# Performance work log

Measured on AMD Instinct MI355X. Metric: run time of the kernel, lower is better.

Reference implementation:

```python
import jax, jax.numpy as jnp
import numpy as np

HEADS = 16
HEAD_DIM = 64
EMBED = HEADS * HEAD_DIM  # 1024
B, S = 2, 2048


def setup_inputs() -> dict:
    key = jax.random.key(0)
    ks = jax.random.split(key, 9)
    return {
        "value": jax.random.normal(ks[0], (B, S, EMBED), dtype=jnp.float32),
        "key": jax.random.normal(ks[1], (B, S, EMBED), dtype=jnp.float32),
        "query": jax.random.normal(ks[2], (B, S, EMBED), dtype=jnp.float32),
        "mask": jax.random.randint(ks[3], (B, 1, S, S), 0, 2, dtype=jnp.int32),
        "Wq": jax.random.normal(ks[4], (HEAD_DIM, HEAD_DIM), dtype=jnp.float32) * 0.02,
        "Wk": jax.random.normal(ks[5], (HEAD_DIM, HEAD_DIM), dtype=jnp.float32) * 0.02,
        "Wv": jax.random.normal(ks[6], (HEAD_DIM, HEAD_DIM), dtype=jnp.float32) * 0.02,
        "Wo": jax.random.normal(ks[7], (EMBED, EMBED), dtype=jnp.float32) * 0.02,
        "bo": jnp.zeros((EMBED,), dtype=jnp.float32),
    }


def reference(value, key, query, mask, Wq, Wk, Wv, Wo, bo):
    N, Lv = value.shape[0], value.shape[1]
    Lk, Lq = key.shape[1], query.shape[1]
    # Faithful to original: plain reshape (N, heads, len, head_dim), NOT transpose.
    v = value.reshape(N, HEADS, Lv, HEAD_DIM)
    k = key.reshape(N, HEADS, Lk, HEAD_DIM)
    q = query.reshape(N, HEADS, Lq, HEAD_DIM)
    # Per-head Linear (no bias): x @ W.T
    V = jnp.einsum('bhld,ed->bhle', v, Wv)
    K = jnp.einsum('bhld,ed->bhle', k, Wk)
    Q = jnp.einsum('bhld,ed->bhle', q, Wq)
    score = jnp.einsum('bhqd,bhkd->bhqk', Q, K)  # [B,H,Sq,Sk]
    score = jnp.where(mask == 0, jnp.float32(-1e20), score)
    # Faithful quirk: scale by sqrt(embed_size), not sqrt(head_dim)
    scale = jnp.float32(EMBED ** 0.5)
    attn = jax.nn.softmax(score / scale, axis=3)
    out = jnp.einsum('bhqk,bhkd->bhqd', attn, V).reshape(N, Lq, HEADS * HEAD_DIM)
    return out @ Wo.T + bo
```

## Files before the change

### kernel.cpp

```cpp
#include <hip/hip_runtime.h>
#include <hip/hip_bf16.h>
#include <cstdint>
#include <cstddef>

#define S_LEN 2048
#define N_HEADS 16
#define HD 64
#define EMB 1024
#define N_BATCH 2
#define N_BH (N_BATCH * N_HEADS)

typedef __attribute__((ext_vector_type(4))) float f32x4;
typedef __attribute__((ext_vector_type(8))) short short8;
typedef __attribute__((ext_vector_type(8))) _Float16 half8;
typedef __attribute__((ext_vector_type(2))) _Float16 half2v;

__device__ __forceinline__ f32x4 mfma16h(half8 a, half8 b, f32x4 c) {
    return __builtin_amdgcn_mfma_f32_16x16x32_f16(a, b, c, 0, 0, 0);
}

__device__ __forceinline__ unsigned pkh(float a, float b) {
    return __builtin_bit_cast(unsigned, __builtin_amdgcn_cvt_pkrtz(a, b));
}

#if __has_builtin(__builtin_amdgcn_exp2f)
__device__ __forceinline__ float fast_exp2(float x) { return __builtin_amdgcn_exp2f(x); }
#else
__device__ __forceinline__ float fast_exp2(float x) { return exp2f(x); }
#endif

__global__ __launch_bounds__(256) void prep_kernel(
    const float* __restrict__ q_in, const float* __restrict__ k_in,
    const float* __restrict__ v_in,
    const float* __restrict__ Wq, const float* __restrict__ Wk,
    const float* __restrict__ Wv, const float* __restrict__ Wo,
    const int* __restrict__ mask,
    short* __restrict__ Qb, short* __restrict__ Kb, short* __restrict__ Vt,
    short* __restrict__ Woh, unsigned long long* __restrict__ bits) {
    __shared__ short Al[64 * 72];
    __shared__ short Wl[64 * 72];
    __shared__ short Ol[64 * 72];
    int bx = blockIdx.x;
    int t = threadIdx.x;

    if (bx >= 3072) {
        if (bx < 11264) {
            int wid = ((bx - 3072) * 256 + t) >> 6;
            int lane = t & 63;
            const int* src = mask + (size_t)wid * 256 + lane;
            unsigned long long w0 = __ballot(src[0] != 0);
            unsigned long long w1 = __ballot(src[64] != 0);
            unsigned long long w2 = __ballot(src[128] != 0);
            unsigned long long w3 = __ballot(src[192] != 0);
            if (lane == 0) {
                unsigned long long* dst = bits + (size_t)wid * 4;
                dst[0] = w0; dst[1] = w1; dst[2] = w2; dst[3] = w3;
            }
        } else {
            int i = (bx - 11264) * 256 + t;
            f32x4 a = reinterpret_cast<const f32x4*>(Wo)[i * 2];
            f32x4 b = reinterpret_cast<const f32x4*>(Wo)[i * 2 + 1];
            uint4 u = { pkh(a.x, a.y), pkh(a.z, a.w), pkh(b.x, b.y), pkh(b.z, b.w) };
            reinterpret_cast<uint4*>(Woh)[i] = u;
        }
        return;
    }

    int rt = bx & 31;
    int bh = (bx >> 5) & 31;
    int tz = bx >> 10;
    const float* src = (tz == 0 ? q_in : tz == 1 ? k_in : v_in)
                       + (size_t)bh * S_LEN * HD + (size_t)rt * 64 * HD;
    const float* W = (tz == 0 ? Wq : tz == 1 ? Wk : Wv);

#pragma unroll
    for (int r = 0; r < 4; r++) {
        int f4 = t + 256 * r;
        int row = f4 >> 4;
        int c4 = (f4 & 15) * 4;
        f32x4 a = reinterpret_cast<const f32x4*>(src)[f4];
        uint2 ua = { pkh(a.x, a.y), pkh(a.z, a.w) };
        *reinterpret_cast<uint2*>(&Al[row * 72 + c4]) = ua;
        f32x4 w = reinterpret_cast<const f32x4*>(W)[f4];
        uint2 uw = { pkh(w.x, w.y), pkh(w.z, w.w) };
        *reinterpret_cast<uint2*>(&Wl[row * 72 + c4]) = uw;
    }
    __syncthreads();

    int wave = t >> 6, lane = t & 63, quad = lane >> 4, col = lane & 15;
    half8 a0 = *reinterpret_cast<const half8*>(&Al[(wave * 16 + col) * 72 + quad * 8]);
    half8 a1 = *reinterpret_cast<const half8*>(&Al[(wave * 16 + col) * 72 + 32 + quad * 8]);

    const float C1 = 0.04508422002777448f;
    float scl = (tz == 0) ? C1 : 1.0f;

    f32x4 acc[4];
#pragma unroll
    for (int jt = 0; jt < 4; jt++) {
        half8 b0 = *reinterpret_cast<const half8*>(&Wl[(jt * 16 + col) * 72 + quad * 8]);
        half8 b1 = *reinterpret_cast<const half8*>(&Wl[(jt * 16 + col) * 72 + 32 + quad * 8]);
        f32x4 c = {0.f, 0.f, 0.f, 0.f};
        c = mfma16h(a0, b0, c);
        c = mfma16h(a1, b1, c);
        acc[jt] = c;
    }
    __syncthreads();

    if (tz < 2) {
#pragma unroll
        for (int jt = 0; jt < 4; jt++)
#pragma unroll
            for (int i = 0; i < 4; i++)
                Ol[(wave * 16 + quad * 4 + i) * 72 + jt * 16 + col] =
                    __builtin_bit_cast(short, (_Float16)(acc[jt][i] * scl));
        __syncthreads();
        short* dst = (tz == 0 ? Qb : Kb) + (size_t)bh * S_LEN * HD + (size_t)rt * 64 * HD;
        int row = t >> 2, ck = (t & 3) * 16;
        short8 o0 = *reinterpret_cast<const short8*>(&Ol[row * 72 + ck]);
        short8 o1 = *reinterpret_cast<const short8*>(&Ol[row * 72 + ck + 8]);
        *reinterpret_cast<short8*>(&dst[row * 64 + ck]) = o0;
        *reinterpret_cast<short8*>(&dst[row * 64 + ck + 8]) = o1;
    } else {
#pragma unroll
        for (int jt = 0; jt < 4; jt++)
#pragma unroll
            for (int i = 0; i < 4; i++)
                Ol[(jt * 16 + col) * 72 + wave * 16 + quad * 4 + i] =
                    __builtin_bit_cast(short, (_Float16)acc[jt][i]);
        __syncthreads();
        short* dst = Vt + (size_t)bh * HD * S_LEN + rt * 64;
        int d = t >> 2, ck = (t & 3) * 16;
        short8 o0 = *reinterpret_cast<const short8*>(&Ol[d * 72 + ck]);
        short8 o1 = *reinterpret_cast<const short8*>(&Ol[d * 72 + ck + 8]);
        *reinterpret_cast<short8*>(&dst[(size_t)d * S_LEN + ck]) = o0;
        *reinterpret_cast<short8*>(&dst[(size_t)d * S_LEN + ck + 8]) = o1;
    }
}

__global__ __launch_bounds__(512, 4) void attn_kernel(
    const short* __restrict__ Qb, const short* __restrict__ Kb,
    const short* __restrict__ Vt, const unsigned long long* __restrict__ mbits,
    short* __restrict__ Xb) {
    int qt = blockIdx.x;
    int bh = blockIdx.y;
    int b = bh >> 4;
    int t = threadIdx.x, wave = t >> 6, lane = t & 63, quad = lane >> 4, col = lane & 15;
    int qg = wave & 3;
    int par = wave >> 2;

    __shared__ short smem[16384 + 8 * 32 * 72];
    short* Pl = smem + 16384;
    short* Pw = Pl + wave * (32 * 72);
    const short* Kp = smem + par * 4096;
    const short* Vp = smem + 8192 + par * 4096;

    const short* Qh = Qb + (size_t)bh * S_LEN * HD;
    const short* Kh = Kb + (size_t)bh * S_LEN * HD;
    const short* Vh = Vt + (size_t)bh * HD * S_LEN;
    int q0 = qt * 128 + qg * 32;

    half8 qf00 = *reinterpret_cast<const half8*>(&Qh[(size_t)(q0 + col) * HD + quad * 8]);
    half8 qf01 = *reinterpret_cast<const half8*>(&Qh[(size_t)(q0 + col) * HD + 32 + quad * 8]);
    half8 qf10 = *reinterpret_cast<const half8*>(&Qh[(size_t)(q0 + 16 + col) * HD + quad * 8]);
    half8 qf11 = *reinterpret_cast<const half8*>(&Qh[(size_t)(q0 + 16 + col) * HD + 32 + quad * 8]);

    const unsigned long long* mrow0 = mbits + (size_t)(b * S_LEN + q0 + col) * 32;
    const unsigned long long* mrow1 = mbits + (size_t)(b * S_LEN + q0 + 16 + col) * 32;

    int r0 = t >> 3, cc = t & 7;
    int dst0 = r0 * 64 + ((cc ^ (r0 & 7)) * 8);
    const short* kg0 = Kh + r0 * HD + cc * 8;
    const short* vg0 = Vh + (size_t)r0 * S_LEN + cc * 8;

    {
        short8 a = *reinterpret_cast<const short8*>(kg0);
        short8 b2 = *reinterpret_cast<const short8*>(kg0 + 4096);
        short8 c = *reinterpret_cast<const short8*>(vg0);
        short8 d = *reinterpret_cast<const short8*>(vg0 + 64);
        *reinterpret_cast<short8*>(&smem[dst0]) = a;
        *reinterpret_cast<short8*>(&smem[4096 + dst0]) = b2;
        *reinterpret_cast<short8*>(&smem[8192 + dst0]) = c;
        *reinterpret_cast<short8*>(&smem[12288 + dst0]) = d;
    }
    __syncthreads();

    unsigned bs[4];
#pragma unroll
    for (int i = 0; i < 4; i++) bs[i] = 1u << (quad * 4 + i);
    half8 ones = { (_Float16)1.f, (_Float16)1.f, (_Float16)1.f, (_Float16)1.f,
                   (_Float16)1.f, (_Float16)1.f, (_Float16)1.f, (_Float16)1.f };

    int sw = quad ^ (col & 7);
    unsigned long long mw0 = mrow0[par];
    unsigned long long mw1 = mrow1[par];

    f32x4 o[4][2];
    f32x4 l0 = {0.f, 0.f, 0.f, 0.f}, l1 = {0.f, 0.f, 0.f, 0.f};
#pragma unroll
    for (int dt = 0; dt < 4; dt++) {
        o[dt][0] = (f32x4){0.f, 0.f, 0.f, 0.f};
        o[dt][1] = (f32x4){0.f, 0.f, 0.f, 0.f};
    }

    for (int s = 0; s < 16; s++) {
        short8 pk0, pk1, pv0, pv1;
        unsigned long long mn0, mn1;
        if (s < 15) {
            pk0 = *reinterpret_cast<const short8*>(kg0 + (2 * s + 2) * 4096);
            pk1 = *reinterpret_cast<const short8*>(kg0 + (2 * s + 3) * 4096);
            pv0 = *reinterpret_cast<const short8*>(vg0 + (2 * s + 2) * 64);
            pv1 = *reinterpret_cast<const short8*>(vg0 + (2 * s + 3) * 64);
            mn0 = mrow0[2 * s + 2 + par];
            mn1 = mrow1[2 * s + 2 + par];
        }
#pragma unroll
        for (int mt = 0; mt < 4; mt++) {
            const short* kbase = &Kp[(mt * 16 + col) * 64];
            half8 ka0 = *reinterpret_cast<const half8*>(&kbase[sw * 8]);
            half8 ka1 = *reinterpret_cast<const half8*>(&kbase[(sw ^ 4) * 8]);
            f32x4 c0 = {0.f, 0.f, 0.f, 0.f};
            f32x4 c1 = {0.f, 0.f, 0.f, 0.f};
            c0 = mfma16h(ka0, qf00, c0);
            c0 = mfma16h(ka1, qf01, c0);
            c1 = mfma16h(ka0, qf10, c1);
            c1 = mfma16h(ka1, qf11, c1);
            unsigned g0 = (unsigned)(mw0 >> (mt * 16));
            unsigned g1 = (unsigned)(mw1 >> (mt * 16));
            float p00 = fast_exp2((g0 & bs[0]) ? c0[0] : -200.0f);
            float p01 = fast_exp2((g0 & bs[1]) ? c0[1] : -200.0f);
            float p02 = fast_exp2((g0 & bs[2]) ? c0[2] : -200.0f);
            float p03 = fast_exp2((g0 & bs[3]) ? c0[3] : -200.0f);
            uint2 dw0 = { pkh(p00, p01), pkh(p02, p03) };
            *reinterpret_cast<uint2*>(&Pw[col * 72 + mt * 16 + quad * 4]) = dw0;
            float p10 = fast_exp2((g1 & bs[0]) ? c1[0] : -200.0f);
            float p11 = fast_exp2((g1 & bs[1]) ? c1[1] : -200.0f);
            float p12 = fast_exp2((g1 & bs[2]) ? c1[2] : -200.0f);
            float p13 = fast_exp2((g1 & bs[3]) ? c1[3] : -200.0f);
            uint2 dw1 = { pkh(p10, p11), pkh(p12, p13) };
            *reinterpret_cast<uint2*>(&Pw[(16 + col) * 72 + mt * 16 + quad * 4]) = dw1;
        }
#pragma unroll
        for (int c = 0; c < 2; c++) {
            half8 pb0 = *reinterpret_cast<const half8*>(&Pw[col * 72 + c * 32 + quad * 8]);
            half8 pb1 = *reinterpret_cast<const half8*>(&Pw[(16 + col) * 72 + c * 32 + quad * 8]);
            l0 = mfma16h(ones, pb0, l0);
            l1 = mfma16h(ones, pb1, l1);
#pragma unroll
            for (int dt = 0; dt < 4; dt++) {
                half8 va = *reinterpret_cast<const half8*>(
                    &Vp[(dt * 16 + col) * 64 + (((c * 4 + quad) ^ (col & 7)) * 8)]);
                o[dt][0] = mfma16h(va, pb0, o[dt][0]);
                o[dt][1] = mfma16h(va, pb1, o[dt][1]);
            }
        }
        __syncthreads();
        if (s < 15) {
            *reinterpret_cast<short8*>(&smem[dst0]) = pk0;
            *reinterpret_cast<short8*>(&smem[4096 + dst0]) = pk1;
            *reinterpret_cast<short8*>(&smem[8192 + dst0]) = pv0;
            *reinterpret_cast<short8*>(&smem[12288 + dst0]) = pv1;
            mw0 = mn0;
            mw1 = mn1;
            __syncthreads();
        }
    }

    float* Obuf = (float*)smem;
    float* Lbuf = (float*)(Pl + 4 * (32 * 72));
    if (par == 1) {
        float* ob = Obuf + qg * 2048 + lane * 32;
#pragma unroll
        for (int dt = 0; dt < 4; dt++) {
            *reinterpret_cast<f32x4*>(&ob[((dt * 2 + 0) ^ (lane & 7)) * 4]) = o[dt][0];
            *reinterpret_cast<f32x4*>(&ob[((dt * 2 + 1) ^ (lane & 7)) * 4]) = o[dt][1];
        }
        if (quad == 0) {
            Lbuf[qg * 32 + col] = l0[0];
            Lbuf[qg * 32 + 16 + col] = l1[0];
        }
    }
    __syncthreads();
    if (par == 0) {
        float* ob = Obuf + qg * 2048 + lane * 32;
        float inv0 = 1.0f / (l0[0] + Lbuf[qg * 32 + col]);
        float inv1 = 1.0f / (l1[0] + Lbuf[qg * 32 + 16 + col]);
#pragma unroll
        for (int dt = 0; dt < 4; dt++) {
            f32x4 a0 = *reinterpret_cast<const f32x4*>(&ob[((dt * 2 + 0) ^ (lane & 7)) * 4]);
            f32x4 a1 = *reinterpret_cast<const f32x4*>(&ob[((dt * 2 + 1) ^ (lane & 7)) * 4]);
            float v00 = (o[dt][0][0] + a0.x) * inv0, v01 = (o[dt][0][1] + a0.y) * inv0;
            float v02 = (o[dt][0][2] + a0.z) * inv0, v03 = (o[dt][0][3] + a0.w) * inv0;
            float v10 = (o[dt][1][0] + a1.x) * inv1, v11 = (o[dt][1][1] + a1.y) * inv1;
            float v12 = (o[dt][1][2] + a1.z) * inv1, v13 = (o[dt][1][3] + a1.w) * inv1;
            uint2 dw0 = { pkh(v00, v01), pkh(v02, v03) };
            uint2 dw1 = { pkh(v10, v11), pkh(v12, v13) };
            *reinterpret_cast<uint2*>(&Pw[col * 72 + dt * 16 + quad * 4]) = dw0;
            *reinterpret_cast<uint2*>(&Pw[(16 + col) * 72 + dt * 16 + quad * 4]) = dw1;
        }
        int rr = lane >> 2, ckk = (lane & 3) * 16;
        short* Xrow = Xb + (size_t)bh * S_LEN * HD + (size_t)(q0 + rr) * HD;
        short8 x0 = *reinterpret_cast<const short8*>(&Pw[rr * 72 + ckk]);
        short8 x1 = *reinterpret_cast<const short8*>(&Pw[rr * 72 + ckk + 8]);
        *reinterpret_cast<short8*>(&Xrow[ckk]) = x0;
        *reinterpret_cast<short8*>(&Xrow[ckk + 8]) = x1;
        short* Xrow2 = Xrow + 16 * HD;
        short8 y0 = *reinterpret_cast<const short8*>(&Pw[(16 + rr) * 72 + ckk]);
        short8 y1 = *reinterpret_cast<const short8*>(&Pw[(16 + rr) * 72 + ckk + 8]);
        *reinterpret_cast<short8*>(&Xrow2[ckk]) = y0;
        *reinterpret_cast<short8*>(&Xrow2[ckk + 8]) = y1;
    }
}

__global__ __launch_bounds__(256, 4) void final_kernel(
    const short* __restrict__ Xb, const short* __restrict__ Woh,
    const float* __restrict__ bo, float* __restrict__ out) {
    int nb = blockIdx.x;
    int mb = blockIdx.y;
    int t = threadIdx.x, wave = t >> 6, lane = t & 63, quad = lane >> 4, col = lane & 15;
    __shared__ short Xs[64 * 64];
    __shared__ short Ws[64 * 64];
    __shared__ float Olds[64 * 68];

    int m0 = mb * 64, n0 = nb * 64;
    int r0 = t >> 3, r1 = (t + 256) >> 3, cc = t & 7;
    int dst0 = r0 * 64 + ((cc ^ (r0 & 7)) * 8);
    int dst1 = r1 * 64 + ((cc ^ (r1 & 7)) * 8);
    const short* xg0 = Xb + (size_t)(m0 + r0) * EMB + cc * 8;
    const short* xg1 = Xb + (size_t)(m0 + r1) * EMB + cc * 8;
    const short* wg0 = Woh + (size_t)(n0 + r0) * EMB + cc * 8;
    const short* wg1 = Woh + (size_t)(n0 + r1) * EMB + cc * 8;

    short8 px0 = *reinterpret_cast<const short8*>(xg0);
    short8 px1 = *reinterpret_cast<const short8*>(xg1);
    short8 pw0 = *reinterpret_cast<const short8*>(wg0);
    short8 pw1 = *reinterpret_cast<const short8*>(wg1);
    *reinterpret_cast<short8*>(&Xs[dst0]) = px0;
    *reinterpret_cast<short8*>(&Xs[dst1]) = px1;
    *reinterpret_cast<short8*>(&Ws[dst0]) = pw0;
    *reinterpret_cast<short8*>(&Ws[dst1]) = pw1;
    __syncthreads();

    int sw = quad ^ (col & 7);
    f32x4 acc[4];
#pragma unroll
    for (int jt = 0; jt < 4; jt++) acc[jt] = (f32x4){0.f, 0.f, 0.f, 0.f};

    for (int s = 0; s < 16; s++) {
        if (s < 15) {
            px0 = *reinterpret_cast<const short8*>(xg0 + (s + 1) * 64);
            px1 = *reinterpret_cast<const short8*>(xg1 + (s + 1) * 64);
            pw0 = *reinterpret_cast<const short8*>(wg0 + (s + 1) * 64);
            pw1 = *reinterpret_cast<const short8*>(wg1 + (s + 1) * 64);
        }
        const short* arow = &Xs[(wave * 16 + col) * 64];
        half8 a0 = *reinterpret_cast<const half8*>(&arow[sw * 8]);
        half8 a1 = *reinterpret_cast<const half8*>(&arow[(sw ^ 4) * 8]);
#pragma unroll
        for (int jt = 0; jt < 4; jt++) {
            const short* brow = &Ws[(jt * 16 + col) * 64];
            half8 b0 = *reinterpret_cast<const half8*>(&brow[sw * 8]);
            half8 b1 = *reinterpret_cast<const half8*>(&brow[(sw ^ 4) * 8]);
            acc[jt] = mfma16h(a0, b0, acc[jt]);
            acc[jt] = mfma16h(a1, b1, acc[jt]);
        }
        __syncthreads();
        if (s < 15) {
            *reinterpret_cast<short8*>(&Xs[dst0]) = px0;
            *reinterpret_cast<short8*>(&Xs[dst1]) = px1;
            *reinterpret_cast<short8*>(&Ws[dst0]) = pw0;
            *reinterpret_cast<short8*>(&Ws[dst1]) = pw1;
            __syncthreads();
        }
    }

#pragma unroll
    for (int jt = 0; jt < 4; jt++)
#pragma unroll
        for (int i = 0; i < 4; i++)
            Olds[(wave * 16 + quad * 4 + i) * 68 + jt * 16 + col] = acc[jt][i];
    __syncthreads();
    int row = t >> 2, ck = (t & 3) * 16;
#pragma unroll
    for (int u = 0; u < 4; u++) {
        f32x4 v = *reinterpret_cast<const f32x4*>(&Olds[row * 68 + ck + u * 4]);
        f32x4 bb = *reinterpret_cast<const f32x4*>(&bo[n0 + ck + u * 4]);
        v.x += bb.x; v.y += bb.y; v.z += bb.z; v.w += bb.w;
        *reinterpret_cast<f32x4*>(&out[(size_t)(m0 + row) * EMB + n0 + ck + u * 4]) = v;
    }
}

extern "C" void kernel_launch(void* const* d_in, const int* in_sizes, int n_in,
                              void* d_out, int out_size, void* d_ws, size_t ws_size,
                              hipStream_t stream) {
    const float* value = (const float*)d_in[0];
    const float* key_  = (const float*)d_in[1];
    const float* query = (const float*)d_in[2];
    const int*   mask  = (const int*)d_in[3];
    const float* Wq = (const float*)d_in[4];
    const float* Wk = (const float*)d_in[5];
    const float* Wv = (const float*)d_in[6];
    const float* Wo = (const float*)d_in[7];
    const float* bo = (const float*)d_in[8];
    float* out = (float*)d_out;

    char* ws = (char*)d_ws;
    short* Qb  = (short*)(ws);
    short* Kb  = (short*)(ws + (size_t)8  * 1048576);
    short* Vt  = (short*)(ws + (size_t)16 * 1048576);
    short* Xb  = (short*)(ws + (size_t)24 * 1048576);
    short* Woh = (short*)(ws + (size_t)32 * 1048576);
    unsigned long long* mbits =
        (unsigned long long*)(ws + (size_t)34 * 1048576);

    prep_kernel<<<dim3(3072 + 8192 + 512), dim3(256), 0, stream>>>(
        query, key_, value, Wq, Wk, Wv, Wo, mask, Qb, Kb, Vt, Woh, mbits);
    attn_kernel<<<dim3(S_LEN / 128, N_BH), dim3(512), 0, stream>>>(Qb, Kb, Vt, mbits, Xb);
    final_kernel<<<dim3(EMB / 64, (N_BATCH * S_LEN) / 64), dim3(256), 0, stream>>>(
        Xb, Woh, bo, out);
}
```

Before: 202.3 us.

## Keep softmax probabilities in registers via permlane32 swap instead of LDS round-trip

Instead of writing the exponentiated probability tile to per-wave LDS and reading it back as MFMA B operands, the packed fp16 values stay in registers and are redistributed with permlane32_swap. To match the new register ordering, the V tile is stored into LDS with a permuted 4-element interleave. This removes LDS writes and reads and a wave-local dependency from the inner loop and shrinks the shared-memory allocation, which may allow more blocks per CU. It relies on the gfx950 permlane32_swap builtin, and the V store becomes twice as many narrower LDS writes.

```diff
diff --git a/kernel.cpp b/kernel.cpp
--- a/kernel.cpp
+++ b/kernel.cpp
@@ -13,7 +13,8 @@
 typedef __attribute__((ext_vector_type(4))) float f32x4;
 typedef __attribute__((ext_vector_type(8))) short short8;
 typedef __attribute__((ext_vector_type(8))) _Float16 half8;
-typedef __attribute__((ext_vector_type(2))) _Float16 half2v;
+typedef __attribute__((ext_vector_type(2))) unsigned uint2v;
+typedef __attribute__((ext_vector_type(4))) unsigned uint4v;
 
 __device__ __forceinline__ f32x4 mfma16h(half8 a, half8 b, f32x4 c) {
     return __builtin_amdgcn_mfma_f32_16x16x32_f16(a, b, c, 0, 0, 0);
@@ -148,9 +149,7 @@
     int qg = wave & 3;
     int par = wave >> 2;
 
-    __shared__ short smem[16384 + 8 * 32 * 72];
-    short* Pl = smem + 16384;
-    short* Pw = Pl + wave * (32 * 72);
+    __shared__ short smem[16384 + 9216 + 256];
     const short* Kp = smem + par * 4096;
     const short* Vp = smem + 8192 + par * 4096;
 
@@ -169,18 +168,24 @@
 
     int r0 = t >> 3, cc = t & 7;
     int dst0 = r0 * 64 + ((cc ^ (r0 & 7)) * 8);
+    int ch0 = cc & ~1;
+    int h4 = (cc & 1) * 4;
+    int vdA = r0 * 64 + ((ch0 ^ (r0 & 7)) * 8) + h4;
+    int vdB = r0 * 64 + (((ch0 + 1) ^ (r0 & 7)) * 8) + h4;
     const short* kg0 = Kh + r0 * HD + cc * 8;
     const short* vg0 = Vh + (size_t)r0 * S_LEN + cc * 8;
 
     {
         short8 a = *reinterpret_cast<const short8*>(kg0);
         short8 b2 = *reinterpret_cast<const short8*>(kg0 + 4096);
-        short8 c = *reinterpret_cast<const short8*>(vg0);
-        short8 d = *reinterpret_cast<const short8*>(vg0 + 64);
+        uint4v uc = __builtin_bit_cast(uint4v, *reinterpret_cast<const short8*>(vg0));
+        uint4v ud = __builtin_bit_cast(uint4v, *reinterpret_cast<const short8*>(vg0 + 64));
         *reinterpret_cast<short8*>(&smem[dst0]) = a;
         *reinterpret_cast<short8*>(&smem[4096 + dst0]) = b2;
-        *reinterpret_cast<short8*>(&smem[8192 + dst0]) = c;
-        *reinterpret_cast<short8*>(&smem[12288 + dst0]) = d;
+        *reinterpret_cast<uint2v*>(&smem[8192 + vdA]) = (uint2v){uc.x, uc.y};
+        *reinterpret_cast<uint2v*>(&smem[8192 + vdB]) = (uint2v){uc.z, uc.w};
+        *reinterpret_cast<uint2v*>(&smem[12288 + vdA]) = (uint2v){ud.x, ud.y};
+        *reinterpret_cast<uint2v*>(&smem[12288 + vdB]) = (uint2v){ud.z, ud.w};
     }
     __syncthreads();
 
@@ -213,6 +218,7 @@
             mn0 = mrow0[2 * s + 2 + par];
             mn1 = mrow1[2 * s + 2 + par];
         }
+        unsigned wA[4][2], wB[4][2];
 #pragma unroll
         for (int mt = 0; mt < 4; mt++) {
             const short* kbase = &Kp[(mt * 16 + col) * 64];
@@ -230,19 +236,23 @@
             float p01 = fast_exp2((g0 & bs[1]) ? c0[1] : -200.0f);
             float p02 = fast_exp2((g0 & bs[2]) ? c0[2] : -200.0f);
             float p03 = fast_exp2((g0 & bs[3]) ? c0[3] : -200.0f);
-            uint2 dw0 = { pkh(p00, p01), pkh(p02, p03) };
-            *reinterpret_cast<uint2*>(&Pw[col * 72 + mt * 16 + quad * 4]) = dw0;
+            wA[mt][0] = pkh(p00, p01);
+            wA[mt][1] = pkh(p02, p03);
             float p10 = fast_exp2((g1 & bs[0]) ? c1[0] : -200.0f);
             float p11 = fast_exp2((g1 & bs[1]) ? c1[1] : -200.0f);
             float p12 = fast_exp2((g1 & bs[2]) ? c1[2] : -200.0f);
             float p13 = fast_exp2((g1 & bs[3]) ? c1[3] : -200.0f);
-            uint2 dw1 = { pkh(p10, p11), pkh(p12, p13) };
-            *reinterpret_cast<uint2*>(&Pw[(16 + col) * 72 + mt * 16 + quad * 4]) = dw1;
+            wB[mt][0] = pkh(p10, p11);
+            wB[mt][1] = pkh(p12, p13);
         }
 #pragma unroll
         for (int c = 0; c < 2; c++) {
-            half8 pb0 = *reinterpret_cast<const half8*>(&Pw[col * 72 + c * 32 + quad * 8]);
-            half8 pb1 = *reinterpret_cast<const half8*>(&Pw[(16 + col) * 72 + c * 32 + quad * 8]);
+            auto ra0 = __builtin_amdgcn_permlane32_swap(wA[2 * c][0], wA[2 * c + 1][0], false, false);
+            auto ra1 = __builtin_amdgcn_permlane32_swap(wA[2 * c][1], wA[2 * c + 1][1], false, false);
+            auto rb0 = __builtin_amdgcn_permlane32_swap(wB[2 * c][0], wB[2 * c + 1][0], false, false);
+            auto rb1 = __builtin_amdgcn_permlane32_swap(wB[2 * c][1], wB[2 * c + 1][1], false, false);
+            half8 pb0 = __builtin_bit_cast(half8, (uint4v){ra0[0], ra1[0], ra0[1], ra1[1]});
+            half8 pb1 = __builtin_bit_cast(half8, (uint4v){rb0[0], rb1[0], rb0[1], rb1[1]});
             l0 = mfma16h(ones, pb0, l0);
             l1 = mfma16h(ones, pb1, l1);
 #pragma unroll
@@ -255,10 +265,14 @@
         }
         __syncthreads();
         if (s < 15) {
+            uint4v u0 = __builtin_bit_cast(uint4v, pv0);
+            uint4v u1 = __builtin_bit_cast(uint4v, pv1);
             *reinterpret_cast<short8*>(&smem[dst0]) = pk0;
             *reinterpret_cast<short8*>(&smem[4096 + dst0]) = pk1;
-            *reinterpret_cast<short8*>(&smem[8192 + dst0]) = pv0;
-            *reinterpret_cast<short8*>(&smem[12288 + dst0]) = pv1;
+            *reinterpret_cast<uint2v*>(&smem[8192 + vdA]) = (uint2v){u0.x, u0.y};
+            *reinterpret_cast<uint2v*>(&smem[8192 + vdB]) = (uint2v){u0.z, u0.w};
+            *reinterpret_cast<uint2v*>(&smem[12288 + vdA]) = (uint2v){u1.x, u1.y};
+            *reinterpret_cast<uint2v*>(&smem[12288 + vdB]) = (uint2v){u1.z, u1.w};
             mw0 = mn0;
             mw1 = mn1;
             __syncthreads();
@@ -266,7 +280,8 @@
     }
 
     float* Obuf = (float*)smem;
-    float* Lbuf = (float*)(Pl + 4 * (32 * 72));
+    short* Ps = smem + 16384;
+    float* Lbuf = (float*)(smem + 16384 + 9216);
     if (par == 1) {
         float* ob = Obuf + qg * 2048 + lane * 32;
 #pragma unroll
@@ -281,6 +296,7 @@
     }
     __syncthreads();
     if (par == 0) {
+        short* Pw = Ps + qg * (32 * 72);
         float* ob = Obuf + qg * 2048 + lane * 32;
         float inv0 = 1.0f / (l0[0] + Lbuf[qg * 32 + col]);
         float inv1 = 1.0f / (l1[0] + Lbuf[qg * 32 + 16 + col]);
```

After: 200.6 us. No clear change (-0.8%).
